# Performance work log

Measured on AMD Instinct MI355X. Metric: run time of the kernel, lower is better.

Reference implementation:

```python
import jax, jax.numpy as jnp
import numpy as np

C = 256; HEADS = 8; LEVELS = 4; POINTS = 4; D = C // HEADS
SPATIAL = np.array([[96, 96], [48, 48], [24, 24], [12, 12]], dtype=np.int32)  # (H, W) per level
AREAS = SPATIAL[:, 0] * SPATIAL[:, 1]
HW = int(AREAS.sum())  # 12240
LSI = np.concatenate([[0], np.cumsum(AREAS)[:-1]]).astype(np.int32)
N = 1; Q = HW


def setup_inputs() -> dict:
    key = jax.random.key(0)
    ks = jax.random.split(key, 12)
    s = 0.02
    return {
        "query": jax.random.normal(ks[0], (N, Q, C), jnp.float32),
        "reference_points": jax.random.uniform(ks[1], (N, Q, LEVELS, 2), jnp.float32),
        "input_flatten": jax.random.normal(ks[2], (N, HW, C), jnp.float32),
        "input_spatial_shapes": jnp.asarray(SPATIAL),
        "input_level_start_index": jnp.asarray(LSI),
        "W_off": jax.random.normal(ks[3], (C, HEADS * LEVELS * POINTS * 2), jnp.float32) * s,
        "b_off": jax.random.normal(ks[4], (HEADS * LEVELS * POINTS * 2,), jnp.float32) * s,
        "W_attn": jax.random.normal(ks[5], (C, HEADS * LEVELS * POINTS), jnp.float32) * s,
        "b_attn": jax.random.normal(ks[6], (HEADS * LEVELS * POINTS,), jnp.float32) * s,
        "W_val": jax.random.normal(ks[7], (C, C), jnp.float32) * (1.0 / np.sqrt(C)),
        "b_val": jax.random.normal(ks[8], (C,), jnp.float32) * s,
        "W_out": jax.random.normal(ks[9], (C, C), jnp.float32) * (1.0 / np.sqrt(C)),
        "b_out": jax.random.normal(ks[10], (C,), jnp.float32) * s,
    }


def _ms_deform_attn(query, reference_points, input_flatten, sp, lsi,
                    W_off, b_off, W_attn, b_attn, W_val, b_val, W_out, b_out):
    n, q, c = query.shape
    hw = input_flatten.shape[1]
    # value projection -> [N, Hd, HW, D]
    value = (input_flatten @ W_val + b_val).reshape(n, hw, HEADS, D).transpose(0, 2, 1, 3)
    # sampling offsets [N,Q,Hd,L,P,2]
    off = (query @ W_off + b_off).reshape(n, q, HEADS, LEVELS, POINTS, 2)
    # attention weights softmaxed over L*P (done inside the fused CUDA kernel)
    attn = jax.nn.softmax((query @ W_attn + b_attn).reshape(n, q, HEADS, LEVELS * POINTS), axis=-1)
    attn = attn.reshape(n, q, HEADS, LEVELS, POINTS)
    # normalized sampling locations (reference_points last dim == 2 branch)
    norm = jnp.stack([sp[:, 1], sp[:, 0]], -1).astype(query.dtype)  # (W, H) per level
    loc = reference_points[:, :, None, :, None, :] + off / norm[None, None, None, :, None, :]
    Hl = sp[:, 0][None, None, None, :, None]
    Wl = sp[:, 1][None, None, None, :, None]
    start = lsi[None, None, None, :, None]
    # grid_sample-style (align_corners=False) pixel coordinates
    x = loc[..., 0] * Wl - 0.5
    y = loc[..., 1] * Hl - 0.5
    x0 = jnp.floor(x); y0 = jnp.floor(y)
    lx = x - x0; ly = y - y0
    x0i = x0.astype(jnp.int32); y0i = y0.astype(jnp.int32)

    def gather(yi, xi):
        valid = (xi >= 0) & (xi < Wl) & (yi >= 0) & (yi < Hl)
        idx = jnp.where(valid, start + yi * Wl + xi, 0)  # [N,Q,Hd,L,P]
        idx_t = idx.transpose(0, 2, 1, 3, 4).reshape(n, HEADS, q * LEVELS * POINTS, 1)
        g = jnp.take_along_axis(value, idx_t, axis=2)  # [N,Hd,Q*L*P,D]
        g = g.reshape(n, HEADS, q, LEVELS, POINTS, D)
        return g * valid.transpose(0, 2, 1, 3, 4)[..., None]

    def w(a):
        return a.transpose(0, 2, 1, 3, 4)[..., None]  # [N,Hd,Q,L,P,1]

    sampled = (gather(y0i, x0i) * w((1 - ly) * (1 - lx))
               + gather(y0i, x0i + 1) * w((1 - ly) * lx)
               + gather(y0i + 1, x0i) * w(ly * (1 - lx))
               + gather(y0i + 1, x0i + 1) * w(ly * lx))  # [N,Hd,Q,L,P,D]
    out = jnp.einsum('nhqlpd,nqhlp->nqhd', sampled, attn).reshape(n, q, c)
    return out @ W_out + b_out


def reference(query, reference_points, input_flatten, input_spatial_shapes, input_level_start_index,
              W_off, b_off, W_attn, b_attn, W_val, b_val, W_out, b_out):
    return _ms_deform_attn(query, reference_points, input_flatten,
                           input_spatial_shapes, input_level_start_index,
                           W_off, b_off, W_attn, b_attn, W_val, b_val, W_out, b_out)
```

## Files before the change

### kernel.cpp

```cpp
#include <hip/hip_runtime.h>

#define QTOT 12240
#define KD   256

typedef float f32x4 __attribute__((ext_vector_type(4)));
typedef short s16x8 __attribute__((ext_vector_type(8)));
typedef unsigned short ushort_t;

__device__ __forceinline__ unsigned short f2b(float x) {
    union { float f; unsigned u; } c; c.f = x;
    unsigned r = c.u + 0x7fffu + ((c.u >> 16) & 1u);
    return (unsigned short)(r >> 16);
}
__device__ __forceinline__ int swz(int row, int kb) { return row * 512 + (kb ^ ((row & 7) << 4)); }

__global__ __launch_bounds__(256) void prep(
    const float* __restrict__ W_val, const float* __restrict__ W_off,
    const float* __restrict__ W_attn, const float* __restrict__ W_out,
    const float* __restrict__ b_off, const float* __restrict__ b_attn,
    ushort_t* __restrict__ WvT, ushort_t* __restrict__ WcT,
    ushort_t* __restrict__ WoT, float* __restrict__ bcomb)
{
    int id = blockIdx.x * 256 + threadIdx.x;
    if (id < 65536) { int n = id >> 8, k = id & 255; WvT[id] = f2b(W_val[k * 256 + n]); }
    else if (id < 163840) {
        int t = id - 65536; int n = t >> 8, k = t & 255;
        float v = (n < 256) ? W_off[k * 256 + n] : W_attn[k * 128 + (n - 256)];
        WcT[t] = f2b(v);
    } else if (id < 229376) {
        int t = id - 163840; int n = t >> 8, k = t & 255;
        WoT[t] = f2b(W_out[k * 256 + n]);
    } else if (id < 229760) {
        int t = id - 229376; bcomb[t] = (t < 256) ? b_off[t] : b_attn[t - 256];
    }
}

__device__ __forceinline__ void stageB_full(const ushort_t* __restrict__ WT, int bn, char* Bs) {
    const int t = threadIdx.x;
    const int n = t >> 2, c0 = (t & 3) * 64;
    const ushort_t* src = WT + (size_t)(bn + n) * KD + c0;
#pragma unroll
    for (int j = 0; j < 8; ++j)
        *(s16x8*)(Bs + swz(n, (c0 + j * 8) * 2)) = *(const s16x8*)(src + j * 8);
}

__device__ __forceinline__ void mm64(char* As, char* Bs, f32x4 (&acc)[2][2]) {
    const int tid = threadIdx.x, lane = tid & 63, wave = tid >> 6;
    const int wr = wave >> 1, wc = wave & 1;
    const int lr = lane & 15, g8 = (lane >> 4) * 8;
#pragma unroll
    for (int kc = 0; kc < 8; ++kc) {
        const int kb = (kc * 32 + g8) * 2;
        s16x8 a0 = *(const s16x8*)(As + swz(wr * 32 + lr,      kb));
        s16x8 a1 = *(const s16x8*)(As + swz(wr * 32 + 16 + lr, kb));
        s16x8 b0 = *(const s16x8*)(Bs + swz(wc * 32 + lr,      kb));
        s16x8 b1 = *(const s16x8*)(Bs + swz(wc * 32 + 16 + lr, kb));
        acc[0][0] = __builtin_amdgcn_mfma_f32_16x16x32_bf16(a0, b0, acc[0][0], 0, 0, 0);
        acc[0][1] = __builtin_amdgcn_mfma_f32_16x16x32_bf16(a0, b1, acc[0][1], 0, 0, 0);
        acc[1][0] = __builtin_amdgcn_mfma_f32_16x16x32_bf16(a1, b0, acc[1][0], 0, 0, 0);
        acc[1][1] = __builtin_amdgcn_mfma_f32_16x16x32_bf16(a1, b1, acc[1][1], 0, 0, 0);
    }
}

__global__ __launch_bounds__(256) void gemm1(
    const float* __restrict__ inflat, const float* __restrict__ query,
    const ushort_t* __restrict__ WvT, const ushort_t* __restrict__ WcT,
    const float* __restrict__ b_val, const float* __restrict__ bcomb,
    ushort_t* __restrict__ projb, ushort_t* __restrict__ offb,
    float* __restrict__ logitf)
{
    __shared__ char As[32768];
    __shared__ char Bs[32768];
    const int bid = blockIdx.x;
    const int linear = (bid & 7) * 240 + (bid >> 3);
    const int mt = linear / 10, nt = linear - mt * 10;
    const int bm = mt * 64;
    const bool isval = nt < 4;
    const int bnc = isval ? nt * 64 : (nt - 4) * 64;

    if (isval) stageB_full(WvT, bnc, Bs);
    else       stageB_full(WcT, bnc, Bs);

    {
        const int t = threadIdx.x;
        const int row = t >> 2, c0 = (t & 3) * 64;
        const int grow = bm + row;
        const float* A = isval ? inflat : query;
        float4 f[16];
        if (grow < QTOT) {
            const float4* s = (const float4*)(A + (size_t)grow * KD + c0);
#pragma unroll
            for (int i = 0; i < 16; ++i) f[i] = s[i];
        } else {
#pragma unroll
            for (int i = 0; i < 16; ++i) f[i] = make_float4(0.f, 0.f, 0.f, 0.f);
        }
#pragma unroll
        for (int j = 0; j < 8; ++j) {
            s16x8 v;
            v[0] = f2b(f[2*j].x);   v[1] = f2b(f[2*j].y);
            v[2] = f2b(f[2*j].z);   v[3] = f2b(f[2*j].w);
            v[4] = f2b(f[2*j+1].x); v[5] = f2b(f[2*j+1].y);
            v[6] = f2b(f[2*j+1].z); v[7] = f2b(f[2*j+1].w);
            *(s16x8*)(As + swz(row, (c0 + j * 8) * 2)) = v;
        }
    }
    __syncthreads();

    f32x4 acc[2][2];
#pragma unroll
    for (int m = 0; m < 2; ++m)
#pragma unroll
        for (int n = 0; n < 2; ++n) acc[m][n] = (f32x4)0.f;
    mm64(As, Bs, acc);

    const int lane = threadIdx.x & 63, wave = threadIdx.x >> 6;
    const int wr = wave >> 1, wc = wave & 1;
    const int lr = lane & 15, rg = (lane >> 4) * 4;
#pragma unroll
    for (int n = 0; n < 2; ++n) {
        const int col = bnc + wc * 32 + n * 16 + lr;
        const float bb = isval ? b_val[col] : bcomb[col];
#pragma unroll
        for (int m = 0; m < 2; ++m)
#pragma unroll
            for (int rr = 0; rr < 4; ++rr) {
                const int row = bm + wr * 32 + m * 16 + rg + rr;
                if (row >= QTOT) continue;
                const float v = acc[m][n][rr] + bb;
                if (isval)          projb[(size_t)row * 256 + col] = f2b(v);
                else if (col < 256) offb [(size_t)row * 256 + col] = f2b(v);
                else                logitf[(size_t)row * 128 + col - 256] = v;
            }
    }
}

__global__ __launch_bounds__(256) void gemm_o(
    const ushort_t* __restrict__ Ab, const ushort_t* __restrict__ WoT,
    const float* __restrict__ b_out, float* __restrict__ out)
{
    __shared__ char As[32768];
    __shared__ char Bs[32768];
    const int bid = blockIdx.x;
    const int linear = (bid & 7) * 96 + (bid >> 3);
    const int mt = linear >> 2, nt = linear & 3;
    const int bm = mt * 64;

    stageB_full(WoT, nt * 64, Bs);

    {
        const int t = threadIdx.x;
        const int row = t >> 2, c0 = (t & 3) * 64;
        const int grow = bm + row;
        if (grow < QTOT) {
            const ushort_t* s = Ab + (size_t)grow * KD + c0;
#pragma unroll
            for (int j = 0; j < 8; ++j)
                *(s16x8*)(As + swz(row, (c0 + j * 8) * 2)) = *(const s16x8*)(s + j * 8);
        } else {
            s16x8 z = (s16x8)0;
#pragma unroll
            for (int j = 0; j < 8; ++j)
                *(s16x8*)(As + swz(row, (c0 + j * 8) * 2)) = z;
        }
    }
    __syncthreads();

    f32x4 acc[2][2];
#pragma unroll
    for (int m = 0; m < 2; ++m)
#pragma unroll
        for (int n = 0; n < 2; ++n) acc[m][n] = (f32x4)0.f;
    mm64(As, Bs, acc);

    const int lane = threadIdx.x & 63, wave = threadIdx.x >> 6;
    const int wr = wave >> 1, wc = wave & 1;
    const int lr = lane & 15, rg = (lane >> 4) * 4;
#pragma unroll
    for (int n = 0; n < 2; ++n) {
        const int col = nt * 64 + wc * 32 + n * 16 + lr;
        const float bb = b_out[col];
#pragma unroll
        for (int m = 0; m < 2; ++m)
#pragma unroll
            for (int rr = 0; rr < 4; ++rr) {
                const int row = bm + wr * 32 + m * 16 + rg + rr;
                if (row < QTOT) out[(size_t)row * 256 + col] = acc[m][n][rr] + bb;
            }
    }
}

__global__ __launch_bounds__(256) void sample4(
    const float* __restrict__ rp, const ushort_t* __restrict__ offb,
    const float* __restrict__ logitf, const ushort_t* __restrict__ projb,
    const int* __restrict__ sp, const int* __restrict__ lsi,
    ushort_t* __restrict__ outpre)
{
    const int bid = blockIdx.x;
    const int qpair = (bid & 7) * 765 + (bid >> 3);
    const int tid = threadIdx.x;
    const int qi = tid >> 7;
    const int q = qpair * 2 + qi;

    __shared__ int   s_idx[256][4];
    __shared__ float s_w[256][4];

    {
        const int t = tid & 127;
        const int l = (t >> 2) & 3;
        float logit = logitf[(size_t)q * 128 + t];
        float mx = logit;
#pragma unroll
        for (int d = 1; d < 16; d <<= 1) mx = fmaxf(mx, __shfl_xor(mx, d));
        float e = __expf(logit - mx);
        float s = e;
#pragma unroll
        for (int d = 1; d < 16; d <<= 1) s += __shfl_xor(s, d);
        const float aw = e / s;

        const unsigned opk = *(const unsigned*)&offb[(size_t)q * 256 + t * 2];
        const float ox = __uint_as_float(opk << 16);
        const float oy = __uint_as_float(opk & 0xffff0000u);

        const int Hl = sp[l * 2], Wl = sp[l * 2 + 1], st = lsi[l];
        const float rx = rp[((size_t)q * 4 + l) * 2 + 0];
        const float ry = rp[((size_t)q * 4 + l) * 2 + 1];

        const float x = rx * (float)Wl + ox - 0.5f;
        const float y = ry * (float)Hl + oy - 0.5f;
        const float xf = floorf(x), yf = floorf(y);
        const int x0 = (int)xf, y0 = (int)yf;
        const float lx = x - xf, ly = y - yf;

        const bool vx0 = (x0 >= 0) && (x0 < Wl);
        const bool vx1 = (x0 + 1 >= 0) && (x0 + 1 < Wl);
        const bool vy0 = (y0 >= 0) && (y0 < Hl);
        const bool vy1 = (y0 + 1 >= 0) && (y0 + 1 < Hl);

        s_w[tid][0] = (vx0 && vy0) ? aw * (1.f - ly) * (1.f - lx) : 0.f;
        s_w[tid][1] = (vx1 && vy0) ? aw * (1.f - ly) * lx         : 0.f;
        s_w[tid][2] = (vx0 && vy1) ? aw * ly * (1.f - lx)         : 0.f;
        s_w[tid][3] = (vx1 && vy1) ? aw * ly * lx                 : 0.f;
        s_idx[tid][0] = (vx0 && vy0) ? (st + y0 * Wl + x0) * 512           : 0;
        s_idx[tid][1] = (vx1 && vy0) ? (st + y0 * Wl + x0 + 1) * 512       : 0;
        s_idx[tid][2] = (vx0 && vy1) ? (st + (y0 + 1) * Wl + x0) * 512     : 0;
        s_idx[tid][3] = (vx1 && vy1) ? (st + (y0 + 1) * Wl + x0 + 1) * 512 : 0;
    }
    __syncthreads();

    const int tt = tid & 127;
    const int h = tt >> 4, qtr = (tt >> 2) & 3, c8 = tt & 3;
    const char* basec = (const char*)projb + (h * 32 + c8 * 8) * 2;

    float a0 = 0, a1 = 0, a2 = 0, a3 = 0, a4 = 0, a5 = 0, a6 = 0, a7 = 0;
#pragma unroll
    for (int p = 0; p < 4; ++p) {
        const int slot = qi * 128 + h * 16 + qtr * 4 + p;
        const int4   id4 = *(const int4*)s_idx[slot];
        const float4 w4  = *(const float4*)s_w[slot];
#pragma unroll
        for (int c = 0; c < 4; ++c) {
            const int   id = (c == 0) ? id4.x : (c == 1) ? id4.y : (c == 2) ? id4.z : id4.w;
            const float w  = (c == 0) ? w4.x  : (c == 1) ? w4.y  : (c == 2) ? w4.z  : w4.w;
            const uint4 v = *(const uint4*)(basec + id);
            a0 += w * __uint_as_float(v.x << 16);
            a1 += w * __uint_as_float(v.x & 0xffff0000u);
            a2 += w * __uint_as_float(v.y << 16);
            a3 += w * __uint_as_float(v.y & 0xffff0000u);
            a4 += w * __uint_as_float(v.z << 16);
            a5 += w * __uint_as_float(v.z & 0xffff0000u);
            a6 += w * __uint_as_float(v.w << 16);
            a7 += w * __uint_as_float(v.w & 0xffff0000u);
        }
    }
    a0 += __shfl_xor(a0, 4); a1 += __shfl_xor(a1, 4);
    a2 += __shfl_xor(a2, 4); a3 += __shfl_xor(a3, 4);
    a4 += __shfl_xor(a4, 4); a5 += __shfl_xor(a5, 4);
    a6 += __shfl_xor(a6, 4); a7 += __shfl_xor(a7, 4);
    a0 += __shfl_xor(a0, 8); a1 += __shfl_xor(a1, 8);
    a2 += __shfl_xor(a2, 8); a3 += __shfl_xor(a3, 8);
    a4 += __shfl_xor(a4, 8); a5 += __shfl_xor(a5, 8);
    a6 += __shfl_xor(a6, 8); a7 += __shfl_xor(a7, 8);

    if (qtr == 0) {
        uint4 o;
        o.x = (unsigned)f2b(a0) | ((unsigned)f2b(a1) << 16);
        o.y = (unsigned)f2b(a2) | ((unsigned)f2b(a3) << 16);
        o.z = (unsigned)f2b(a4) | ((unsigned)f2b(a5) << 16);
        o.w = (unsigned)f2b(a6) | ((unsigned)f2b(a7) << 16);
        *(uint4*)&outpre[(size_t)q * 256 + h * 32 + c8 * 8] = o;
    }
}

extern "C" void kernel_launch(void* const* d_in, const int* in_sizes, int n_in,
                              void* d_out, int out_size, void* d_ws, size_t ws_size,
                              hipStream_t stream) {
    const float* query  = (const float*)d_in[0];
    const float* rp     = (const float*)d_in[1];
    const float* inflat = (const float*)d_in[2];
    const int*   sp     = (const int*)d_in[3];
    const int*   lsi    = (const int*)d_in[4];
    const float* W_off  = (const float*)d_in[5];
    const float* b_off  = (const float*)d_in[6];
    const float* W_attn = (const float*)d_in[7];
    const float* b_attn = (const float*)d_in[8];
    const float* W_val  = (const float*)d_in[9];
    const float* b_val  = (const float*)d_in[10];
    const float* W_out  = (const float*)d_in[11];
    const float* b_out  = (const float*)d_in[12];
    float* out = (float*)d_out;

    char* ws = (char*)d_ws;
    ushort_t* projb  = (ushort_t*)ws; ws += (size_t)QTOT * 256 * 2;
    ushort_t* offb   = (ushort_t*)ws; ws += (size_t)QTOT * 256 * 2;
    float*    logitf = (float*)ws;    ws += (size_t)QTOT * 128 * 4;
    ushort_t* outpre = (ushort_t*)ws; ws += (size_t)QTOT * 256 * 2;
    ushort_t* WvT    = (ushort_t*)ws; ws += 65536 * 2;
    ushort_t* WcT    = (ushort_t*)ws; ws += 98304 * 2;
    ushort_t* WoT    = (ushort_t*)ws; ws += 65536 * 2;
    float*    bcomb  = (float*)ws;    ws += 384 * 4;

    dim3 blk(256);

    prep<<<dim3(898), blk, 0, stream>>>(W_val, W_off, W_attn, W_out, b_off, b_attn,
                                        WvT, WcT, WoT, bcomb);

    gemm1<<<dim3(1920), blk, 0, stream>>>(inflat, query, WvT, WcT, b_val, bcomb,
                                          projb, offb, logitf);

    sample4<<<dim3(6120), blk, 0, stream>>>(rp, offb, logitf, projb, sp, lsi, outpre);

    gemm_o<<<dim3(768), blk, 0, stream>>>(outpre, WoT, b_out, out);
}
```

Before: 82.77 us.

## Load weight fragments directly into registers, drop B shared-memory staging in GEMMs

Both GEMM kernels now have each wave own 16 output columns. The wave loads its B fragments for all of K straight from global memory into registers, so the 32 KB B shared buffer and its staging stores are gone. gemm_o also reads A fragments directly from global memory with no LDS and no barrier, clamping rows past the end. This cuts LDS use, which can raise occupancy, and removes a sync. In exchange, every wave re-reads A rows from global or L2 memory, and the B loads per lane are uncoalesced 16-byte strided accesses.

```diff
diff --git a/kernel.cpp b/kernel.cpp
--- a/kernel.cpp
+++ b/kernel.cpp
@@ -35,33 +35,6 @@
     }
 }
 
-__device__ __forceinline__ void stageB_full(const ushort_t* __restrict__ WT, int bn, char* Bs) {
-    const int t = threadIdx.x;
-    const int n = t >> 2, c0 = (t & 3) * 64;
-    const ushort_t* src = WT + (size_t)(bn + n) * KD + c0;
-#pragma unroll
-    for (int j = 0; j < 8; ++j)
-        *(s16x8*)(Bs + swz(n, (c0 + j * 8) * 2)) = *(const s16x8*)(src + j * 8);
-}
-
-__device__ __forceinline__ void mm64(char* As, char* Bs, f32x4 (&acc)[2][2]) {
-    const int tid = threadIdx.x, lane = tid & 63, wave = tid >> 6;
-    const int wr = wave >> 1, wc = wave & 1;
-    const int lr = lane & 15, g8 = (lane >> 4) * 8;
-#pragma unroll
-    for (int kc = 0; kc < 8; ++kc) {
-        const int kb = (kc * 32 + g8) * 2;
-        s16x8 a0 = *(const s16x8*)(As + swz(wr * 32 + lr,      kb));
-        s16x8 a1 = *(const s16x8*)(As + swz(wr * 32 + 16 + lr, kb));
-        s16x8 b0 = *(const s16x8*)(Bs + swz(wc * 32 + lr,      kb));
-        s16x8 b1 = *(const s16x8*)(Bs + swz(wc * 32 + 16 + lr, kb));
-        acc[0][0] = __builtin_amdgcn_mfma_f32_16x16x32_bf16(a0, b0, acc[0][0], 0, 0, 0);
-        acc[0][1] = __builtin_amdgcn_mfma_f32_16x16x32_bf16(a0, b1, acc[0][1], 0, 0, 0);
-        acc[1][0] = __builtin_amdgcn_mfma_f32_16x16x32_bf16(a1, b0, acc[1][0], 0, 0, 0);
-        acc[1][1] = __builtin_amdgcn_mfma_f32_16x16x32_bf16(a1, b1, acc[1][1], 0, 0, 0);
-    }
-}
-
 __global__ __launch_bounds__(256) void gemm1(
     const float* __restrict__ inflat, const float* __restrict__ query,
     const ushort_t* __restrict__ WvT, const ushort_t* __restrict__ WcT,
@@ -70,124 +43,131 @@
     float* __restrict__ logitf)
 {
     __shared__ char As[32768];
-    __shared__ char Bs[32768];
     const int bid = blockIdx.x;
     const int linear = (bid & 7) * 240 + (bid >> 3);
     const int mt = linear / 10, nt = linear - mt * 10;
     const int bm = mt * 64;
     const bool isval = nt < 4;
     const int bnc = isval ? nt * 64 : (nt - 4) * 64;
-
-    if (isval) stageB_full(WvT, bnc, Bs);
-    else       stageB_full(WcT, bnc, Bs);
-
+    const ushort_t* WT = isval ? WvT : WcT;
+    const float* A = isval ? inflat : query;
+
+    const int tid = threadIdx.x, lane = tid & 63, wave = tid >> 6;
+    const int lr = lane & 15, g8 = (lane >> 4) * 8;
+
+    s16x8 bfr[8];
     {
-        const int t = threadIdx.x;
-        const int row = t >> 2, c0 = (t & 3) * 64;
+        const ushort_t* bp = WT + (size_t)(bnc + wave * 16 + lr) * KD + g8;
+#pragma unroll
+        for (int kc = 0; kc < 8; ++kc) bfr[kc] = *(const s16x8*)(bp + kc * 32);
+    }
+
+    {
+        const int row = tid >> 2, c0 = (tid & 3) * 64;
         const int grow = bm + row;
-        const float* A = isval ? inflat : query;
-        float4 f[16];
         if (grow < QTOT) {
-            const float4* s = (const float4*)(A + (size_t)grow * KD + c0);
-#pragma unroll
-            for (int i = 0; i < 16; ++i) f[i] = s[i];
+            const float4* src = (const float4*)(A + (size_t)grow * KD + c0);
+#pragma unroll
+            for (int j = 0; j < 4; ++j) {
+                float4 f0 = src[j * 4 + 0], f1 = src[j * 4 + 1];
+                float4 f2 = src[j * 4 + 2], f3 = src[j * 4 + 3];
+                s16x8 v0, v1;
+                v0[0] = f2b(f0.x); v0[1] = f2b(f0.y); v0[2] = f2b(f0.z); v0[3] = f2b(f0.w);
+                v0[4] = f2b(f1.x); v0[5] = f2b(f1.y); v0[6] = f2b(f1.z); v0[7] = f2b(f1.w);
+                v1[0] = f2b(f2.x); v1[1] = f2b(f2.y); v1[2] = f2b(f2.z); v1[3] = f2b(f2.w);
+                v1[4] = f2b(f3.x); v1[5] = f2b(f3.y); v1[6] = f2b(f3.z); v1[7] = f2b(f3.w);
+                *(s16x8*)(As + swz(row, (c0 + j * 16) * 2))     = v0;
+                *(s16x8*)(As + swz(row, (c0 + j * 16 + 8) * 2)) = v1;
+            }
         } else {
-#pragma unroll
-            for (int i = 0; i < 16; ++i) f[i] = make_float4(0.f, 0.f, 0.f, 0.f);
-        }
-#pragma unroll
-        for (int j = 0; j < 8; ++j) {
-            s16x8 v;
-            v[0] = f2b(f[2*j].x);   v[1] = f2b(f[2*j].y);
-            v[2] = f2b(f[2*j].z);   v[3] = f2b(f[2*j].w);
-            v[4] = f2b(f[2*j+1].x); v[5] = f2b(f[2*j+1].y);
-            v[6] = f2b(f[2*j+1].z); v[7] = f2b(f[2*j+1].w);
-            *(s16x8*)(As + swz(row, (c0 + j * 8) * 2)) = v;
+            s16x8 z = (s16x8)0;
+#pragma unroll
+            for (int j = 0; j < 8; ++j)
+                *(s16x8*)(As + swz(row, (c0 + j * 8) * 2)) = z;
         }
     }
     __syncthreads();
 
-    f32x4 acc[2][2];
-#pragma unroll
-    for (int m = 0; m < 2; ++m)
-#pragma unroll
-        for (int n = 0; n < 2; ++n) acc[m][n] = (f32x4)0.f;
-    mm64(As, Bs, acc);
-
-    const int lane = threadIdx.x & 63, wave = threadIdx.x >> 6;
-    const int wr = wave >> 1, wc = wave & 1;
-    const int lr = lane & 15, rg = (lane >> 4) * 4;
-#pragma unroll
-    for (int n = 0; n < 2; ++n) {
-        const int col = bnc + wc * 32 + n * 16 + lr;
-        const float bb = isval ? b_val[col] : bcomb[col];
-#pragma unroll
-        for (int m = 0; m < 2; ++m)
-#pragma unroll
-            for (int rr = 0; rr < 4; ++rr) {
-                const int row = bm + wr * 32 + m * 16 + rg + rr;
-                if (row >= QTOT) continue;
-                const float v = acc[m][n][rr] + bb;
-                if (isval)          projb[(size_t)row * 256 + col] = f2b(v);
-                else if (col < 256) offb [(size_t)row * 256 + col] = f2b(v);
-                else                logitf[(size_t)row * 128 + col - 256] = v;
-            }
-    }
+    f32x4 acc[4];
+#pragma unroll
+    for (int mf = 0; mf < 4; ++mf) acc[mf] = (f32x4)0.f;
+
+#pragma unroll
+    for (int kc = 0; kc < 8; ++kc) {
+        const int kb = (kc * 32 + g8) * 2;
+#pragma unroll
+        for (int mf = 0; mf < 4; ++mf) {
+            s16x8 af = *(const s16x8*)(As + swz(mf * 16 + lr, kb));
+            acc[mf] = __builtin_amdgcn_mfma_f32_16x16x32_bf16(af, bfr[kc], acc[mf], 0, 0, 0);
+        }
+    }
+
+    const int rg = (lane >> 4) * 4;
+    const int col = bnc + wave * 16 + lr;
+    const float bb = isval ? b_val[col] : bcomb[col];
+#pragma unroll
+    for (int mf = 0; mf < 4; ++mf)
+#pragma unroll
+        for (int rr = 0; rr < 4; ++rr) {
+            const int row = bm + mf * 16 + rg + rr;
+            if (row >= QTOT) continue;
+            const float v = acc[mf][rr] + bb;
+            if (isval)          projb[(size_t)row * 256 + col] = f2b(v);
+            else if (col < 256) offb [(size_t)row * 256 + col] = f2b(v);
+            else                logitf[(size_t)row * 128 + col - 256] = v;
+        }
 }
 
 __global__ __launch_bounds__(256) void gemm_o(
     const ushort_t* __restrict__ Ab, const ushort_t* __restrict__ WoT,
     const float* __restrict__ b_out, float* __restrict__ out)
 {
-    __shared__ char As[32768];
-    __shared__ char Bs[32768];
     const int bid = blockIdx.x;
     const int linear = (bid & 7) * 96 + (bid >> 3);
     const int mt = linear >> 2, nt = linear & 3;
     const int bm = mt * 64;
 
-    stageB_full(WoT, nt * 64, Bs);
-
+    const int tid = threadIdx.x, lane = tid & 63, wave = tid >> 6;
+    const int lr = lane & 15, g8 = (lane >> 4) * 8;
+
+    s16x8 bfr[8];
     {
-        const int t = threadIdx.x;
-        const int row = t >> 2, c0 = (t & 3) * 64;
-        const int grow = bm + row;
-        if (grow < QTOT) {
-            const ushort_t* s = Ab + (size_t)grow * KD + c0;
-#pragma unroll
-            for (int j = 0; j < 8; ++j)
-                *(s16x8*)(As + swz(row, (c0 + j * 8) * 2)) = *(const s16x8*)(s + j * 8);
-        } else {
-            s16x8 z = (s16x8)0;
-#pragma unroll
-            for (int j = 0; j < 8; ++j)
-                *(s16x8*)(As + swz(row, (c0 + j * 8) * 2)) = z;
-        }
-    }
-    __syncthreads();
-
-    f32x4 acc[2][2];
-#pragma unroll
-    for (int m = 0; m < 2; ++m)
-#pragma unroll
-        for (int n = 0; n < 2; ++n) acc[m][n] = (f32x4)0.f;
-    mm64(As, Bs, acc);
-
-    const int lane = threadIdx.x & 63, wave = threadIdx.x >> 6;
-    const int wr = wave >> 1, wc = wave & 1;
-    const int lr = lane & 15, rg = (lane >> 4) * 4;
-#pragma unroll
-    for (int n = 0; n < 2; ++n) {
-        const int col = nt * 64 + wc * 32 + n * 16 + lr;
-        const float bb = b_out[col];
-#pragma unroll
-        for (int m = 0; m < 2; ++m)
-#pragma unroll
-            for (int rr = 0; rr < 4; ++rr) {
-                const int row = bm + wr * 32 + m * 16 + rg + rr;
-                if (row < QTOT) out[(size_t)row * 256 + col] = acc[m][n][rr] + bb;
-            }
-    }
+        const ushort_t* bp = WoT + (size_t)(nt * 64 + wave * 16 + lr) * KD + g8;
+#pragma unroll
+        for (int kc = 0; kc < 8; ++kc) bfr[kc] = *(const s16x8*)(bp + kc * 32);
+    }
+
+    const ushort_t* ap[4];
+#pragma unroll
+    for (int mf = 0; mf < 4; ++mf) {
+        int r = bm + mf * 16 + lr;
+        if (r >= QTOT) r = QTOT - 1;
+        ap[mf] = Ab + (size_t)r * KD + g8;
+    }
+
+    f32x4 acc[4];
+#pragma unroll
+    for (int mf = 0; mf < 4; ++mf) acc[mf] = (f32x4)0.f;
+
+#pragma unroll
+    for (int kc = 0; kc < 8; ++kc) {
+#pragma unroll
+        for (int mf = 0; mf < 4; ++mf) {
+            s16x8 af = *(const s16x8*)(ap[mf] + kc * 32);
+            acc[mf] = __builtin_amdgcn_mfma_f32_16x16x32_bf16(af, bfr[kc], acc[mf], 0, 0, 0);
+        }
+    }
+
+    const int rg = (lane >> 4) * 4;
+    const int col = nt * 64 + wave * 16 + lr;
+    const float bb = b_out[col];
+#pragma unroll
+    for (int mf = 0; mf < 4; ++mf)
+#pragma unroll
+        for (int rr = 0; rr < 4; ++rr) {
+            const int row = bm + mf * 16 + rg + rr;
+            if (row < QTOT) out[(size_t)row * 256 + col] = acc[mf][rr] + bb;
+        }
 }
 
 __global__ __launch_bounds__(256) void sample4(
```

Result: no change. 81.88 us (-1.1%).
